# Kernel optimization log

Hardware: AMD Instinct MI355X
Metric: run time of the kernel (lower is better)

Reference implementation:

```python
import jax, jax.numpy as jnp
import numpy as np

B, C, H, W = 4, 64, 256, 256
WS = 8          # window size
HEADS = 4       # dim // dim_head, dim_head = 16
DH = 16         # dim_head used for scale
HID = 64        # gated conv FFN hidden (mult=1)


def conv2d(x, w, b=None, stride=1, pad=1, groups=1):
    out = jax.lax.conv_general_dilated(
        x, w, (stride, stride), [(pad, pad), (pad, pad)],
        feature_group_count=groups,
        dimension_numbers=('NCHW', 'OIHW', 'NCHW'))
    if b is not None:
        out = out + b[None, :, None, None]
    return out


def gelu(x):
    return jax.nn.gelu(x, approximate=False)  # torch F.gelu / nn.GELU default (erf)


def ln2d(x, w, b, eps=1e-6):  # LayerNorm2d: normalize over channel dim
    mu = jnp.mean(x, axis=1, keepdims=True)
    var = jnp.mean((x - mu) ** 2, axis=1, keepdims=True)
    return w[None, :, None, None] * ((x - mu) / jnp.sqrt(var + eps)) + b[None, :, None, None]


def ln_last(x, w, b, eps=1e-5):  # nn.LayerNorm over last dim
    mu = jnp.mean(x, axis=-1, keepdims=True)
    var = jnp.mean((x - mu) ** 2, axis=-1, keepdims=True)
    return w * ((x - mu) / jnp.sqrt(var + eps)) + b


def to_windows(x, w):  # b d (x w1) (y w2) -> b x y w1 w2 d
    b, c, h, ww = x.shape
    x = x.reshape(b, c, h // w, w, ww // w, w)
    return jnp.transpose(x, (0, 2, 4, 3, 5, 1))


def from_windows(x):  # b x y w1 w2 d -> b d (x w1) (y w2)
    b, nx, ny, w1, w2, c = x.shape
    return jnp.transpose(x, (0, 5, 1, 3, 2, 4)).reshape(b, c, nx * w1, ny * w2)


def setup_inputs() -> dict:
    key = jax.random.key(0)
    ks = iter(jax.random.split(key, 64))

    def rn(*shape):
        return jax.random.normal(next(ks), shape, dtype=jnp.float32) * 0.05

    d = dict(
        x=jax.random.normal(next(ks), (B, C, H, W), dtype=jnp.float32),
        norm_w=jnp.ones((C,), jnp.float32), norm_b=jnp.zeros((C,), jnp.float32),
        conv1_w=rn(C, C, 1, 1), conv1_b=jnp.zeros((C,), jnp.float32),
        conv2_w=rn(C, 2 * C, 1, 1), conv2_b=jnp.zeros((C,), jnp.float32),
        mb_w1=rn(C, C, 1, 1), mb_b1=jnp.zeros((C,), jnp.float32),
        mb_dw_w=rn(C, 1, 3, 3), mb_dw_b=jnp.zeros((C,), jnp.float32),
        se_w1=rn(16, C), se_w2=rn(C, 16),
        mb_w2=rn(C, C, 1, 1), mb_b2=jnp.zeros((C,), jnp.float32),
        ln_att_w=jnp.ones((C,), jnp.float32), ln_att_b=jnp.zeros((C,), jnp.float32),
        q1_w=rn(C // 2, C), q1_b=jnp.zeros((C // 2,), jnp.float32),
        qkv_w=rn(3 * C // 2, C // 2),
        to_out_w=rn(C // 2, C // 2),
        sr_w=rn(C, C, 3, 3), sr_b=jnp.zeros((C,), jnp.float32),
        ln_sr_w=jnp.ones((C,), jnp.float32), ln_sr_b=jnp.zeros((C,), jnp.float32),
        kv1_w=rn(C, C), kv1_b=jnp.zeros((C,), jnp.float32),
        q2_w=rn(C // 2, C), q2_b=jnp.zeros((C // 2,), jnp.float32),
        cd_w=rn(C // 2, C // 2, 3, 3), cd_b=jnp.zeros((C // 2,), jnp.float32),
        cu_w=rn(C // 2, C // 2, 3, 3), cu_b=jnp.zeros((C // 2,), jnp.float32),
        cln1_w=jnp.ones((C,), jnp.float32), cln1_b=jnp.zeros((C,), jnp.float32),
        ff1_in_w=rn(2 * HID, C, 1, 1), ff1_dw_w=rn(2 * HID, 1, 3, 3), ff1_out_w=rn(C, HID, 1, 1),
        cln2_w=jnp.ones((C,), jnp.float32), cln2_b=jnp.zeros((C,), jnp.float32),
        ca_temp=jnp.ones((HEADS, 1, 1), jnp.float32),
        ca_qkv_w=rn(3 * C, C, 1, 1), ca_dw_w=rn(3 * C, 1, 3, 3), ca_out_w=rn(C, C, 1, 1),
        cln3_w=jnp.ones((C,), jnp.float32), cln3_b=jnp.zeros((C,), jnp.float32),
        ff2_in_w=rn(2 * HID, C, 1, 1), ff2_dw_w=rn(2 * HID, 1, 3, 3), ff2_out_w=rn(C, HID, 1, 1),
    )
    return d


def reference(x, norm_w, norm_b, conv1_w, conv1_b, conv2_w, conv2_b,
              mb_w1, mb_b1, mb_dw_w, mb_dw_b, se_w1, se_w2, mb_w2, mb_b2,
              ln_att_w, ln_att_b, q1_w, q1_b, qkv_w, to_out_w,
              sr_w, sr_b, ln_sr_w, ln_sr_b, kv1_w, kv1_b, q2_w, q2_b,
              cd_w, cd_b, cu_w, cu_b,
              cln1_w, cln1_b, ff1_in_w, ff1_dw_w, ff1_out_w,
              cln2_w, cln2_b, ca_temp, ca_qkv_w, ca_dw_w, ca_out_w,
              cln3_w, cln3_b, ff2_in_w, ff2_dw_w, ff2_out_w):
    scale = DH ** -0.5
    # input norm + 1x1 conv
    y = conv2d(ln2d(x, norm_w, norm_b), conv1_w, conv1_b, pad=0)
    # ---- MBConv (expansion 1, SE, residual) ----
    r = y
    t = gelu(conv2d(y, mb_w1, mb_b1, pad=0))
    t = gelu(conv2d(t, mb_dw_w, mb_dw_b, pad=1, groups=C))
    s = jnp.mean(t, axis=(2, 3))                      # (B,C) squeeze
    s = jax.nn.sigmoid(jax.nn.silu(s @ se_w1.T) @ se_w2.T)
    y = conv2d(t * s[:, :, None, None], mb_w2, mb_b2, pad=0) + r
    # ---- windowed hybrid attention, PreNormResidual ----
    xw = to_windows(y, WS)                            # (B,nx,ny,8,8,C)
    xn = ln_last(xw, ln_att_w, ln_att_b)
    xf = from_windows(xn)                             # (B,C,H,W)
    b, c, h, w = xf.shape
    nx, ny = h // WS, w // WS
    # window self-attention branch on dim/2
    xq = jnp.einsum('bchw,oc->bohw', xf, q1_w) + q1_b[None, :, None, None]
    tw = to_windows(xq, WS).reshape(b * nx * ny, WS * WS, c // 2)
    qkv = tw @ qkv_w.T
    q, k, v = jnp.split(qkv, 3, axis=-1)

    def heads_split(t):
        return jnp.transpose(t.reshape(t.shape[0], WS * WS, HEADS, -1), (0, 2, 1, 3))

    q, k, v = heads_split(q) * scale, heads_split(k), heads_split(v)
    attn = jax.nn.softmax(jnp.einsum('bhid,bhjd->bhij', q, k), axis=-1)
    o = jnp.einsum('bhij,bhjd->bhid', attn, v)
    o = jnp.transpose(o, (0, 2, 1, 3)).reshape(b * nx * ny, WS, WS, c // 2)
    o = (o @ to_out_w.T).reshape(b, nx, ny, WS, WS, c // 2)
    # low-resolution cross-attention branch on dim/2
    iq = jnp.einsum('bchw,oc->bohw', xf, q2_w) + q2_b[None, :, None, None]
    iq = conv2d(iq, cd_w, cd_b, stride=8, pad=1)      # (B,C/2,H/8,W/8)
    qq = jnp.transpose(iq.reshape(b, h * w // 64, HEADS // 2, c // HEADS), (0, 2, 1, 3))
    x1 = conv2d(xf, sr_w, sr_b, stride=16, pad=1)     # (B,C,h16,w16)
    x1 = jnp.transpose(x1.reshape(b, c, -1), (0, 2, 1))
    x1 = gelu(ln_last(x1, ln_sr_w, ln_sr_b))
    kv = (x1 @ kv1_w.T + kv1_b).reshape(b, -1, 2, HEADS // 2, c // HEADS)
    kv = jnp.transpose(kv, (2, 0, 3, 1, 4))
    k1, v1 = kv[0], kv[1]                             # (B,2,N,16)
    a1 = jax.nn.softmax(jnp.einsum('bhid,bhjd->bhij', qq, k1) * scale, axis=-1)
    o1 = jnp.einsum('bhij,bhjd->bhid', a1, v1)        # (B,2,HW/64,16)
    o1 = jnp.transpose(o1, (0, 1, 3, 2)).reshape(b, c // 2, h // 8, w // 8)
    o1 = jnp.repeat(jnp.repeat(o1, 8, axis=2), 8, axis=3)   # nearest upsample x8
    o1 = to_windows(conv2d(o1, cu_w, cu_b, pad=1), WS)
    xw = jnp.concatenate([o, o1], axis=-1) + xw       # residual
    y = from_windows(xw)

    def gcff(z, in_w, dw_w, out_w):
        t = conv2d(conv2d(z, in_w, pad=0), dw_w, pad=1, groups=2 * HID)
        a, g = jnp.split(t, 2, axis=1)
        return conv2d(gelu(a) * g, out_w, pad=0)

    y = y + gcff(ln2d(y, cln1_w, cln1_b), ff1_in_w, ff1_dw_w, ff1_out_w)
    # ---- windowed channel (transposed) attention ----
    z = ln2d(y, cln2_w, cln2_b)
    qkv2 = conv2d(conv2d(z, ca_qkv_w, pad=0), ca_dw_w, pad=1, groups=3 * C)
    qc, kc, vc = jnp.split(qkv2, 3, axis=1)
    hp, wp = h // WS, w // WS

    def rw(t):  # b (head d) (h ph) (w pw) -> b (h w) head d (ph pw)
        t = t.reshape(b, HEADS, C // HEADS, hp, WS, wp, WS)
        return jnp.transpose(t, (0, 3, 5, 1, 2, 4, 6)).reshape(b, hp * wp, HEADS, C // HEADS, WS * WS)

    qc, kc, vc = rw(qc), rw(kc), rw(vc)
    qc = qc / jnp.clip(jnp.linalg.norm(qc, axis=-1, keepdims=True), 1e-12)
    kc = kc / jnp.clip(jnp.linalg.norm(kc, axis=-1, keepdims=True), 1e-12)
    aat = jax.nn.softmax(jnp.einsum('bnhde,bnhfe->bnhdf', qc, kc) * ca_temp, axis=-1)
    oc = jnp.einsum('bnhdf,bnhfe->bnhde', aat, vc)    # (B,Nw,head,16,64)
    oc = oc.reshape(b, hp, wp, HEADS, C // HEADS, WS, WS)
    oc = jnp.transpose(oc, (0, 3, 4, 1, 5, 2, 6)).reshape(b, C, h, w)
    y = y + conv2d(oc, ca_out_w, pad=0)
    y = y + gcff(ln2d(y, cln3_w, cln3_b), ff2_in_w, ff2_dw_w, ff2_out_w)
    # fuse branch with block input
    return conv2d(jnp.concatenate([x, y], axis=1), conv2_w, conv2_b, pad=0)
```

## Files before the change

### kernel.cpp

```cpp
#include <hip/hip_runtime.h>
#include <hip/hip_bf16.h>
#include <math.h>

typedef __hip_bfloat16 bf16;

static constexpr int B_ = 4;
static constexpr int C_ = 64;
static constexpr int H_ = 256;
static constexpr int W_ = 256;
static constexpr int P_ = H_ * W_;
static constexpr int NP_ = B_ * P_;

static constexpr int HSTR = 61;

__device__ __forceinline__ float cvt(float x) { return x; }
__device__ __forceinline__ float cvt(bf16 x) { return __bfloat162float(x); }
__device__ __forceinline__ float geluf(float x) { return 0.5f * x * (1.0f + erff(x * 0.70710678118654752f)); }
__device__ __forceinline__ float sigm(float x) { return 1.0f / (1.0f + __expf(-x)); }

__device__ __forceinline__ float ldin(const void* p, int i, bool bf) {
    return bf ? __bfloat162float(((const bf16*)p)[i]) : ((const float*)p)[i];
}

__device__ __forceinline__ void bf2x(unsigned u, float& a, float& b) {
// ... 105 lines not shown
    int p = g & (P_ - 1);
    int base = bb * C_ * P_ + p;
    float v[C_];
    float mu = 0.f;
#pragma unroll
    for (int c = 0; c < C_; ++c) { v[c] = in[base + c * P_]; mu += v[c]; }
    mu *= (1.0f / C_);
    float var = 0.f;
#pragma unroll
    for (int c = 0; c < C_; ++c) { float d = v[c] - mu; var += d * d; }
    var *= (1.0f / C_);
    float inv = rsqrtf(var + eps);
#pragma unroll
    for (int c = 0; c < C_; ++c)
        out[base + c * P_] = __float2bfloat16((v[c] - mu) * inv * swt[c] + sbt[c]);
}

template <int COUT>
__global__ __launch_bounds__(256) void k_pwln(const float* __restrict__ Yin,
                                              const void* __restrict__ lnw, const void* __restrict__ lnb,
                                              const void* __restrict__ w,
                                              bf16* __restrict__ out,
                                              const int* __restrict__ dtf) {
    const bool bf = dtf[0] != 0;
    __shared__ bf16 swb[COUT * 64];
    __shared__ float slw[64], slb[64];
    for (int i = threadIdx.x; i < COUT * 64; i += 256) swb[i] = __float2bfloat16(ldin(w, i, bf));
    if (threadIdx.x < 64) {
        slw[threadIdx.x] = ldin(lnw, threadIdx.x, bf);
        slb[threadIdx.x] = ldin(lnb, threadIdx.x, bf);
    }
    __syncthreads();
    int g = blockIdx.x * 256 + threadIdx.x;
    int bb = g >> 16, p = g & (P_ - 1);
    int base = bb * 64 * P_ + p;
    float v[64];
    float mu = 0.f;
#pragma unroll
    for (int c = 0; c < 64; ++c) { v[c] = Yin[base + c * P_]; mu += v[c]; }
    mu *= (1.0f / 64.0f);
    float var = 0.f;
#pragma unroll
    for (int c = 0; c < 64; ++c) { float d = v[c] - mu; var += d * d; }
    float inv = rsqrtf(var * (1.0f / 64.0f) + 1e-6f);
#pragma unroll
    for (int c = 0; c < 64; ++c) v[c] = (v[c] - mu) * inv * slw[c] + slb[c];
    int obase = bb * COUT * P_ + p;
    const unsigned* uw = (const unsigned*)swb;
    for (int o = 0; o < COUT; ++o) {
        float a = 0.f;
#pragma unroll
        for (int cc = 0; cc < 32; ++cc) {
            float wa, wb;
            bf2x(uw[o * 32 + cc], wa, wb);
            a = fmaf(wa, v[2 * cc], fmaf(wb, v[2 * cc + 1], a));
        }
        out[obase + o * P_] = __float2bfloat16(a);
    }
}

__global__ __launch_bounds__(256) void k_dwmean(const bf16* __restrict__ h,
                                                const void* __restrict__ dww,
                                                const void* __restrict__ dwb,
                                                float* __restrict__ part,
                                                const int* __restrict__ dtf) {
    const bool bf = dtf[0] != 0;
    __shared__ __align__(8) bf16 hsb[10 * 256];
    __shared__ float red[256];
    int bid = blockIdx.x;
    int bc = bid >> 5, chunk = bid & 31;
    int c = bc & 63;
    int h0 = chunk * 8;
    int base = bc * P_;
    int tid = threadIdx.x;
    {
        const unsigned* gq = (const unsigned*)h;
        unsigned* hu = (unsigned*)hsb;
        for (int i = tid; i < 1280; i += 256) {
            int r = i >> 7, col2 = i & 127;
            int hh = h0 - 1 + r;
            unsigned v = 0u;
            if ((unsigned)hh < (unsigned)H_) v = gq[(base + hh * W_) / 2 + col2];
            hu[r * 128 + col2] = v;
        }
    }
    float w9[9];
#pragma unroll
    for (int k = 0; k < 9; ++k) w9[k] = ldin(dww, c * 9 + k, bf);
    float bv = ldin(dwb, c, bf);
    __syncthreads();
    float acc = 0.f;
#pragma unroll
    for (int k = 0; k < 8; ++k) {
        int j = tid + k * 256;
        int r = j >> 8, x = j & 255;
        float s = bv;
#pragma unroll
        for (int kh = 0; kh < 3; ++kh) {
            const bf16* row = &hsb[(r + kh) * 256];
            float vm1 = (x > 0) ? cvt(row[x - 1]) : 0.f;
            float v0 = cvt(row[x]);
            float vp1 = (x < 255) ? cvt(row[x + 1]) : 0.f;
            s = fmaf(w9[kh * 3 + 0], vm1, s);
            s = fmaf(w9[kh * 3 + 1], v0, s);
            s = fmaf(w9[kh * 3 + 2], vp1, s);
        }
        acc += geluf(s);
    }
    red[tid] = acc;
    __syncthreads();
    for (int s2 = 128; s2 > 0; s2 >>= 1) {
        if (tid < s2) red[tid] += red[tid + s2];
        __syncthreads();
    }
    if (tid == 0) part[bc * 32 + chunk] = red[0];
}

__global__ __launch_bounds__(256) void k_se(const float* __restrict__ part,
                                            const void* __restrict__ w1,
                                            const void* __restrict__ w2,
                                            float* __restrict__ sfin,
                                            const int* __restrict__ dtf) {
    const bool bf = dtf[0] != 0;
    __shared__ float ssum[256];
    __shared__ float hbuf[B_ * 16];
    int t = threadIdx.x;
    {
        float a = 0.f;
#pragma unroll
        for (int k = 0; k < 32; ++k) a += part[t * 32 + k];
        ssum[t] = a * (1.0f / P_);
    }
    __syncthreads();
    if (t < B_ * 16) {
        int bb = t >> 4, j = t & 15;
        float a = 0.f;
        for (int c = 0; c < 64; ++c) a = fmaf(ssum[bb * 64 + c], ldin(w1, j * 64 + c, bf), a);
        hbuf[t] = a * sigm(a);
    }
    __syncthreads();
    int bb = t >> 6, c = t & 63;
    float a = 0.f;
    for (int j = 0; j < 16; ++j) a = fmaf(hbuf[bb * 16 + j], ldin(w2, c * 16 + j, bf), a);
    sfin[t] = sigm(a);
}

__global__ __launch_bounds__(256) void k_mb2w(const bf16* __restrict__ h,
                                              const void* __restrict__ dww, const void* __restrict__ dwb,
                                              const void* __restrict__ w2, const void* __restrict__ b2,
                                              const float* __restrict__ sfin,
                                              float* __restrict__ Y,
                                              const int* __restrict__ dtf) {
    const bool bf = dtf[0] != 0;
    __shared__ __align__(16) char arena[24832];
    unsigned* hsu = (unsigned*)arena;
    bf16* ts = (bf16*)(arena + 15616);
    float* sdb = (float*)(arena + 24064);
    float* sb2 = (float*)(arena + 24320);
    float* ssc = (float*)(arena + 24576);
    bf16* sw2T = (bf16*)arena;
    int wid = win_swz(blockIdx.x);
    int bb = wid >> 10;
    int h0 = ((wid >> 5) & 31) * 8, w0 = (wid & 31) * 8;
    int tid = threadIdx.x;
    int cch = tid >> 2, quarter = tid & 3;
    {
        const unsigned* gq = (const unsigned*)h;
        int j = quarter * 15;
        int pr = j / 6, col = j - pr * 6;
        size_t chb = (size_t)(bb * 64 + cch) * P_;
        for (int k = 0; k < 15; ++k) {
            int hh = h0 + pr - 1;
            int wcx = w0 - 2 + 2 * col;
            unsigned v = 0u;
            if ((unsigned)hh < (unsigned)H_ && (unsigned)wcx < 255u)
                v = gq[(chb + hh * W_ + wcx) >> 1];
            hsu[cch * HSTR + j] = v;
            ++j; ++col;
            if (col == 6) { col = 0; ++pr; }
        }
    }
    float w9[9];
#pragma unroll
    for (int k = 0; k < 9; ++k) w9[k] = ldin(dww, cch * 9 + k, bf);
    if (tid < 64) {
        sdb[tid] = ldin(dwb, tid, bf);
        sb2[tid] = ldin(b2, tid, bf);
        ssc[tid] = sfin[bb * 64 + tid];
    }
    __syncthreads();
    {
        const unsigned* mua = hsu + cch * HSTR;
        unsigned* tsu = (unsigned*)ts;
        float bv = sdb[cch];
        float sc = ssc[cch];
#pragma unroll
        for (int k = 0; k < 8; ++k) {
            int p = quarter * 8 + k;
            int t0 = 2 * p;
            int rt = t0 >> 3, ct = t0 & 7;
            float a0 = bv, a1 = bv;
#pragma unroll
            for (int kh = 0; kh < 3; ++kh) {
                int rb = (rt + kh) * 6 + (ct >> 1);
                unsigned u0 = mua[rb], u1 = mua[rb + 1], u2 = mua[rb + 2];
                float x1 = bfhi(u0);
                float x2 = bflo(u1), x3 = bfhi(u1);
                float x4 = bflo(u2);
                a0 = fmaf(w9[kh * 3 + 0], x1, fmaf(w9[kh * 3 + 1], x2, fmaf(w9[kh * 3 + 2], x3, a0)));
                a1 = fmaf(w9[kh * 3 + 0], x2, fmaf(w9[kh * 3 + 1], x3, fmaf(w9[kh * 3 + 2], x4, a1)));
            }
            tsu[cch * 33 + p] = bfpack(geluf(a0) * sc, geluf(a1) * sc);
        }
    }
    __syncthreads();
    for (int i = tid; i < 4096; i += 256) {
        int c = i >> 6, o = i & 63;
        sw2T[c * 64 + o] = __float2bfloat16(ldin(w2, o * 64 + c, bf));
    }
    __syncthreads();
    int og = tid >> 4, pg = tid & 15;
    int o0 = og * 4, p0 = pg * 4;
    float acc[4][4] = {};
    const unsigned* wt = (const unsigned*)sw2T;
    const unsigned* tt = (const unsigned*)ts;
    for (int c = 0; c < 64; ++c) {
        float w0v, w1v, w2v, w3v, t0, t1, t2, t3;
        bf2x(wt[c * 32 + (o0 >> 1)], w0v, w1v);
        bf2x(wt[c * 32 + (o0 >> 1) + 1], w2v, w3v);
        bf2x(tt[c * 33 + (p0 >> 1)], t0, t1);
        bf2x(tt[c * 33 + (p0 >> 1) + 1], t2, t3);
        acc[0][0] = fmaf(w0v, t0, acc[0][0]); acc[0][1] = fmaf(w0v, t1, acc[0][1]);
        acc[0][2] = fmaf(w0v, t2, acc[0][2]); acc[0][3] = fmaf(w0v, t3, acc[0][3]);
        acc[1][0] = fmaf(w1v, t0, acc[1][0]); acc[1][1] = fmaf(w1v, t1, acc[1][1]);
        acc[1][2] = fmaf(w1v, t2, acc[1][2]); acc[1][3] = fmaf(w1v, t3, acc[1][3]);
        acc[2][0] = fmaf(w2v, t0, acc[2][0]); acc[2][1] = fmaf(w2v, t1, acc[2][1]);
        acc[2][2] = fmaf(w2v, t2, acc[2][2]); acc[2][3] = fmaf(w2v, t3, acc[2][3]);
        acc[3][0] = fmaf(w3v, t0, acc[3][0]); acc[3][1] = fmaf(w3v, t1, acc[3][1]);
        acc[3][2] = fmaf(w3v, t2, acc[3][2]); acc[3][3] = fmaf(w3v, t3, acc[3][3]);
    }
#pragma unroll
    for (int i = 0; i < 4; ++i)
#pragma unroll
        for (int j = 0; j < 4; ++j) {
            int t = p0 + j;
            int p = (h0 + (t >> 3)) * W_ + w0 + (t & 7);
            Y[(bb * 64 + o0 + i) * P_ + p] += acc[i][j] + sb2[o0 + i];
        }
}

__global__ __launch_bounds__(256) void k_wprep(const void* __restrict__ q1w, const void* __restrict__ q1b,
                                               const void* __restrict__ qkvw, const void* __restrict__ outw,
                                               bf16* __restrict__ WQT, float* __restrict__ BQ,
                                               bf16* __restrict__ OWT,
                                               const int* __restrict__ dtf) {
    const bool bf = dtf[0] != 0;
    __shared__ float sq1[32 * 64];
    __shared__ float sqk[96 * 32];
    __shared__ float sb1[32];
    int tid = threadIdx.x;
    for (int i = tid; i < 2048; i += 256) sq1[i] = ldin(q1w, i, bf);
    for (int i = tid; i < 3072; i += 256) sqk[i] = ldin(qkvw, i, bf);
    if (tid < 32) sb1[tid] = ldin(q1b, tid, bf);
    __syncthreads();
    for (int idx = tid; idx < 6144; idx += 256) {
        int o = idx % 96, c = idx / 96;
        float a = 0.f;
        for (int k = 0; k < 32; ++k) a = fmaf(sqk[o * 32 + k], sq1[k * 64 + c], a);
        if (o < 32) a *= 0.25f;
        WQT[c * 96 + o] = __float2bfloat16(a);
    }
    if (tid < 96) {
        float a = 0.f;
        for (int k = 0; k < 32; ++k) a = fmaf(sqk[tid * 32 + k], sb1[k], a);
        if (tid < 32) a *= 0.25f;
        BQ[tid] = a;
    }
    for (int idx = tid; idx < 1024; idx += 256) {
        int o = idx >> 5, c = idx & 31;
        OWT[c * 32 + o] = __float2bfloat16(ldin(outw, o * 32 + c, bf));
    }
}

__global__ __launch_bounds__(256, 4) void k_winattn(const bf16* __restrict__ xf,
                                                    const uint4* __restrict__ WQT,
                                                    const float* __restrict__ BQ,
                                                    const unsigned* __restrict__ OWT,
                                                    float* __restrict__ Y) {
    __shared__ __align__(16) char arena[35200];
    int wid = win_swz(blockIdx.x);
    int bb = wid >> 10;
    int h0 = ((wid >> 5) & 31) * 8, w0 = (wid & 31) * 8;
    int tid = threadIdx.x;
    {
        uint4* sW4 = (uint4*)arena;
        for (int i = tid; i < 768; i += 256) sW4[i] = WQT[i];
        if (tid < 96) ((float*)(arena + 12288))[tid] = BQ[tid];
#pragma unroll
        for (int k = 0; k < 2; ++k) {
            int idx = tid + k * 256;
            int c = idx >> 3, r = idx & 7;
            const uint4 v = *(const uint4*)(xf + (size_t)(bb * 64 + c) * P_ + (h0 + r) * W_ + w0);
            *(uint4*)(arena + 12672 + c * 144 + r * 16) = v;
        }
    }
    __syncthreads();
    {
        const unsigned* uW = (const unsigned*)arena;
        const float* sbq = (const float*)(arena + 12288);
        const unsigned* uX = (const unsigned*)(arena + 12672);
        unsigned* uQw = (unsigned*)(arena + 21888);
        int og = tid >> 4, pg = tid & 15;
        float acc[6][4];
#pragma unroll
        for (int i = 0; i < 6; ++i) {
            float b = sbq[og * 6 + i];
#pragma unroll
            for (int j = 0; j < 4; ++j) acc[i][j] = b;
        }
        for (int c = 0; c < 64; ++c) {
            unsigned wu0 = uW[c * 48 + 3 * og];
            unsigned wu1 = uW[c * 48 + 3 * og + 1];
            unsigned wu2 = uW[c * 48 + 3 * og + 2];
            unsigned xu0 = uX[c * 36 + 2 * pg];
            unsigned xu1 = uX[c * 36 + 2 * pg + 1];
            float wv[6], xv[4];
            bf2x(wu0, wv[0], wv[1]); bf2x(wu1, wv[2], wv[3]); bf2x(wu2, wv[4], wv[5]);
            bf2x(xu0, xv[0], xv[1]); bf2x(xu1, xv[2], xv[3]);
#pragma unroll
            for (int i = 0; i < 6; ++i)
#pragma unroll
                for (int j = 0; j < 4; ++j) acc[i][j] = fmaf(wv[i], xv[j], acc[i][j]);
        }
#pragma unroll
        for (int j = 0; j < 4; ++j) {
            int t = pg * 4 + j;
#pragma unroll
            for (int k = 0; k < 3; ++k) {
                union { unsigned u; bf16 h[2]; } pk;
                pk.h[0] = __float2bfloat16(acc[2 * k][j]);
                pk.h[1] = __float2bfloat16(acc[2 * k + 1][j]);
                uQw[t * 52 + 3 * og + k] = pk.u;
            }
        }
    }
    __syncthreads();
    {
        int hH = tid >> 6, lane = tid & 63;
        const unsigned* uQ = (const unsigned*)(arena + 21888);
        unsigned ow0 = OWT[tid * 2], ow1 = OWT[tid * 2 + 1];
        float qf[8];
        {
            const uint4 qv = *(const uint4*)&uQ[lane * 52 + hH * 4];
            bf2x(qv.x, qf[0], qf[1]); bf2x(qv.y, qf[2], qf[3]);
            bf2x(qv.z, qf[4], qf[5]); bf2x(qv.w, qf[6], qf[7]);
        }
        float p[64];
#pragma unroll
        for (int j = 0; j < 64; ++j) {
            const uint4 kv4 = *(const uint4*)&uQ[j * 52 + 16 + hH * 4];
            float kf[8];
            bf2x(kv4.x, kf[0], kf[1]); bf2x(kv4.y, kf[2], kf[3]);
            bf2x(kv4.z, kf[4], kf[5]); bf2x(kv4.w, kf[6], kf[7]);
            float s = 0.f;
#pragma unroll
            for (int d = 0; d < 8; ++d) s = fmaf(qf[d], kf[d], s);
            p[j] = s;
        }
        float m0 = fmaxf(p[0], p[4]), m1 = fmaxf(p[1], p[5]);
        float m2 = fmaxf(p[2], p[6]), m3 = fmaxf(p[3], p[7]);
#pragma unroll
// ... 98 lines not shown
    int bb = g / (OS * OS * COUT);
    float acc = ldin(bias, oc, bf);
    for (int ic = 0; ic < CIN; ++ic) {
        int ibase = (bb * CIN + ic) * P_;
        int wbase = (oc * CIN + ic) * 9;
#pragma unroll
        for (int kh = 0; kh < 3; ++kh) {
            int ih = oh * STRIDE + kh - 1;
            if ((unsigned)ih >= (unsigned)H_) continue;
#pragma unroll
            for (int kw = 0; kw < 3; ++kw) {
                int iw = ow * STRIDE + kw - 1;
                if ((unsigned)iw >= (unsigned)W_) continue;
                acc = fmaf(ldin(w, wbase + kh * 3 + kw, bf), cvt(in[ibase + ih * W_ + iw]), acc);
            }
        }
    }
    out[g] = acc;
}

__global__ __launch_bounds__(64) void k_srkv(const float* __restrict__ x1,
                                             const void* __restrict__ lnw,
                                             const void* __restrict__ lnb,
                                             const void* __restrict__ kvw,
                                             const void* __restrict__ kvb,
                                             float* __restrict__ k1,
                                             float* __restrict__ v1,
                                             const int* __restrict__ dtf) {
    const bool bf = dtf[0] != 0;
    int tok = blockIdx.x;
    int bb = tok >> 8;
    int n = tok & 255;
    int c = threadIdx.x;
    __shared__ float sv[64];
    __shared__ float sg[64];
    float v = x1[(bb * 64 + c) * 256 + n];
    sv[c] = v;
    __syncthreads();
    float mu = 0.f;
    for (int i = 0; i < 64; ++i) mu += sv[i];
    mu *= (1.0f / 64.0f);
    float var = 0.f;
    for (int i = 0; i < 64; ++i) { float d = sv[i] - mu; var += d * d; }
    var *= (1.0f / 64.0f);
    float xn = (v - mu) * rsqrtf(var + 1e-5f) * ldin(lnw, c, bf) + ldin(lnb, c, bf);
    sg[c] = geluf(xn);
    __syncthreads();
    float acc = ldin(kvb, c, bf);
    for (int j = 0; j < 64; ++j) acc = fmaf(ldin(kvw, c * 64 + j, bf), sg[j], acc);
    int kk = c >> 5;
    int jh = (c >> 4) & 1;
    int d = c & 15;
    float* dst = kk ? v1 : k1;
    dst[((bb * 2 + jh) * 256 + n) * 16 + d] = acc;
}

__global__ __launch_bounds__(256) void k_xattn(const float* __restrict__ iqd,
                                               const float* __restrict__ k1,
                                               const float* __restrict__ v1,
                                               float* __restrict__ o1sp) {
    int bid = blockIdx.x;
    int iblk = bid & 3;
    int j = (bid >> 2) & 1;
    int bb = bid >> 3;
    __shared__ float sk[256 * 16];
    __shared__ float svv[256 * 16];
    int kbase = ((bb * 2 + j) * 256) * 16;
    for (int idx = threadIdx.x; idx < 4096; idx += 256) { sk[idx] = k1[kbase + idx]; svv[idx] = v1[kbase + idx]; }
    __syncthreads();
    int i = iblk * 256 + threadIdx.x;
    float q[16];
    int qbase = ((bb * 32 + (i >> 5)) * 32 + (i & 31)) * 32 + j * 16;
#pragma unroll
    for (int d = 0; d < 16; ++d) q[d] = iqd[qbase + d];
    float m = -1e30f, l = 0.f, o[16];
#pragma unroll
    for (int d = 0; d < 16; ++d) o[d] = 0.f;
    for (int n = 0; n < 256; ++n) {
        float s = 0.f;
#pragma unroll
        for (int d = 0; d < 16; ++d) s = fmaf(q[d], sk[n * 16 + d], s);
        s *= 0.25f;
        float mn = fmaxf(m, s);
        float corr = __expf(m - mn);
        float e = __expf(s - mn);
        l = l * corr + e;
#pragma unroll
        for (int d = 0; d < 16; ++d) o[d] = fmaf(o[d], corr, e * svv[n * 16 + d]);
        m = mn;
    }
    float r = 1.0f / l;
#pragma unroll
    for (int d = 0; d < 16; ++d)
        o1sp[((bb * 32 + j * 16 + d) * 32 + (i >> 5)) * 32 + (i & 31)] = o[d] * r;
}

__global__ __launch_bounds__(256) void k_cuconv(const float* __restrict__ o1sp,
                                                const void* __restrict__ w,
                                                const void* __restrict__ bias,
                                                float* __restrict__ Y,
                                                const int* __restrict__ dtf) {
    const bool bf = dtf[0] != 0;
    __shared__ float sw[32 * 32 * 9];
    for (int i = threadIdx.x; i < 9216; i += 256) sw[i] = ldin(w, i, bf);
    __syncthreads();
    int g = blockIdx.x * 256 + threadIdx.x;
    int bb = g >> 16;
    int p = g & 65535;
    int h = p >> 8, x = p & 255;
    float acc[32];
#pragma unroll
    for (int oc = 0; oc < 32; ++oc) acc[oc] = ldin(bias, oc, bf);
    for (int ic = 0; ic < 32; ++ic) {
        int ibase = (bb * 32 + ic) * 1024;
        float v[9];
#pragma unroll
        for (int kh = 0; kh < 3; ++kh)
#pragma unroll
            for (int kw = 0; kw < 3; ++kw) {
                int hh = h + kh - 1, ww = x + kw - 1;
                v[kh * 3 + kw] = ((unsigned)hh < (unsigned)H_ && (unsigned)ww < (unsigned)W_)
                                     ? o1sp[ibase + (hh >> 3) * 32 + (ww >> 3)] : 0.f;
            }
        for (int oc = 0; oc < 32; ++oc) {
            const float* wr = &sw[(oc * 32 + ic) * 9];
            float a = acc[oc];
#pragma unroll
            for (int k = 0; k < 9; ++k) a = fmaf(wr[k], v[k], a);
            acc[oc] = a;
        }
    }
#pragma unroll
    for (int oc = 0; oc < 32; ++oc) Y[(bb * 64 + 32 + oc) * P_ + p] += acc[oc];
}

__global__ __launch_bounds__(256) void k_gcff2(const bf16* __restrict__ mid_g,
                                               const void* __restrict__ dww,
                                               const void* __restrict__ outw,
                                               float* __restrict__ Y,
                                               const int* __restrict__ dtf) {
    const bool bf = dtf[0] != 0;
    __shared__ __align__(16) char arena[24064];
    unsigned* cbu = (unsigned*)arena;
    bf16* ts = (bf16*)(arena + 15616);
    bf16* sowT = (bf16*)arena;
    int wid = win_swz(blockIdx.x);
    int bb = wid >> 10;
    int h0 = ((wid >> 5) & 31) * 8, w0 = (wid & 31) * 8;
    int tid = threadIdx.x;
    int cch = tid >> 2, quarter = tid & 3;
    int j0 = quarter * 15;
    int pr0 = j0 / 6, col0 = j0 - pr0 * 6;
    const unsigned* gq = (const unsigned*)mid_g;
    float areg[16];
    float w9[9];
    {
        int j = j0, pr = pr0, col = col0;
        size_t chb = (size_t)(bb * 128 + cch) * P_;
        for (int k = 0; k < 15; ++k) {
            int hh = h0 + pr - 1;
            int wcx = w0 - 2 + 2 * col;
            unsigned v = 0u;
            if ((unsigned)hh < (unsigned)H_ && (unsigned)wcx < 255u)
                v = gq[(chb + hh * W_ + wcx) >> 1];
            cbu[cch * HSTR + j] = v;
            ++j; ++col;
            if (col == 6) { col = 0; ++pr; }
        }
    }
#pragma unroll
    for (int k = 0; k < 9; ++k) w9[k] = ldin(dww, cch * 9 + k, bf);
    __syncthreads();
    {
        const unsigned* mua = cbu + cch * HSTR;
#pragma unroll
        for (int k = 0; k < 8; ++k) {
            int p = quarter * 8 + k;
            int t0 = 2 * p;
            int rt = t0 >> 3, ct = t0 & 7;
            float a0 = 0.f, a1 = 0.f;
#pragma unroll
            for (int kh = 0; kh < 3; ++kh) {
                int rb = (rt + kh) * 6 + (ct >> 1);
                unsigned u0 = mua[rb], u1 = mua[rb + 1], u2 = mua[rb + 2];
                float x1 = bfhi(u0);
                float x2 = bflo(u1), x3 = bfhi(u1);
                float x4 = bflo(u2);
                a0 = fmaf(w9[kh * 3 + 0], x1, fmaf(w9[kh * 3 + 1], x2, fmaf(w9[kh * 3 + 2], x3, a0)));
                a1 = fmaf(w9[kh * 3 + 0], x2, fmaf(w9[kh * 3 + 1], x3, fmaf(w9[kh * 3 + 2], x4, a1)));
            }
            areg[2 * k] = a0;
            areg[2 * k + 1] = a1;
        }
    }
    __syncthreads();
    {
        int j = j0, pr = pr0, col = col0;
        size_t chb = (size_t)(bb * 128 + 64 + cch) * P_;
        for (int k = 0; k < 15; ++k) {
            int hh = h0 + pr - 1;
            int wcx = w0 - 2 + 2 * col;
            unsigned v = 0u;
            if ((unsigned)hh < (unsigned)H_ && (unsigned)wcx < 255u)
                v = gq[(chb + hh * W_ + wcx) >> 1];
            cbu[cch * HSTR + j] = v;
            ++j; ++col;
            if (col == 6) { col = 0; ++pr; }
        }
    }
#pragma unroll
    for (int k = 0; k < 9; ++k) w9[k] = ldin(dww, (64 + cch) * 9 + k, bf);
    __syncthreads();
    {
        const unsigned* mua = cbu + cch * HSTR;
        unsigned* tsu = (unsigned*)ts;
#pragma unroll
        for (int k = 0; k < 8; ++k) {
            int p = quarter * 8 + k;
            int t0 = 2 * p;
            int rt = t0 >> 3, ct = t0 & 7;
            float g0 = 0.f, g1 = 0.f;
#pragma unroll
            for (int kh = 0; kh < 3; ++kh) {
                int rb = (rt + kh) * 6 + (ct >> 1);
                unsigned u0 = mua[rb], u1 = mua[rb + 1], u2 = mua[rb + 2];
                float x1 = bfhi(u0);
                float x2 = bflo(u1), x3 = bfhi(u1);
                float x4 = bflo(u2);
                g0 = fmaf(w9[kh * 3 + 0], x1, fmaf(w9[kh * 3 + 1], x2, fmaf(w9[kh * 3 + 2], x3, g0)));
                g1 = fmaf(w9[kh * 3 + 0], x2, fmaf(w9[kh * 3 + 1], x3, fmaf(w9[kh * 3 + 2], x4, g1)));
            }
            tsu[cch * 33 + p] = bfpack(geluf(areg[2 * k]) * g0, geluf(areg[2 * k + 1]) * g1);
        }
    }
    __syncthreads();
    for (int i = tid; i < 4096; i += 256) {
        int c = i >> 6, o = i & 63;
        sowT[c * 64 + o] = __float2bfloat16(ldin(outw, o * 64 + c, bf));
    }
    __syncthreads();
    int og = tid >> 4, pg = tid & 15;
    int o0 = og * 4, p0 = pg * 4;
    float acc[4][4] = {};
    const unsigned* wt = (const unsigned*)sowT;
    const unsigned* tt = (const unsigned*)ts;
    for (int c = 0; c < 64; ++c) {
        float w0v, w1v, w2v, w3v, t0, t1, t2, t3;
        bf2x(wt[c * 32 + (o0 >> 1)], w0v, w1v);
        bf2x(wt[c * 32 + (o0 >> 1) + 1], w2v, w3v);
        bf2x(tt[c * 33 + (p0 >> 1)], t0, t1);
        bf2x(tt[c * 33 + (p0 >> 1) + 1], t2, t3);
        acc[0][0] = fmaf(w0v, t0, acc[0][0]); acc[0][1] = fmaf(w0v, t1, acc[0][1]);
        acc[0][2] = fmaf(w0v, t2, acc[0][2]); acc[0][3] = fmaf(w0v, t3, acc[0][3]);
        acc[1][0] = fmaf(w1v, t0, acc[1][0]); acc[1][1] = fmaf(w1v, t1, acc[1][1]);
        acc[1][2] = fmaf(w1v, t2, acc[1][2]); acc[1][3] = fmaf(w1v, t3, acc[1][3]);
        acc[2][0] = fmaf(w2v, t0, acc[2][0]); acc[2][1] = fmaf(w2v, t1, acc[2][1]);
        acc[2][2] = fmaf(w2v, t2, acc[2][2]); acc[2][3] = fmaf(w2v, t3, acc[2][3]);
        acc[3][0] = fmaf(w3v, t0, acc[3][0]); acc[3][1] = fmaf(w3v, t1, acc[3][1]);
        acc[3][2] = fmaf(w3v, t2, acc[3][2]); acc[3][3] = fmaf(w3v, t3, acc[3][3]);
    }
#pragma unroll
    for (int i = 0; i < 4; ++i)
#pragma unroll
        for (int j = 0; j < 4; ++j) {
            int t = p0 + j;
            int p = (h0 + (t >> 3)) * W_ + w0 + (t & 7);
            Y[(bb * 64 + o0 + i) * P_ + p] += acc[i][j];
        }
}

__global__ __launch_bounds__(256) void k_chattn2(const bf16* __restrict__ qkv_g,
                                                 const void* __restrict__ dww,
                                                 const void* __restrict__ outw,
                                                 const void* __restrict__ tempw,
                                                 float* __restrict__ Y,
                                                 const int* __restrict__ dtf) {
    const bool bf = dtf[0] != 0;
    __shared__ __align__(16) char arena[40960];
    bf16* sq = (bf16*)arena;
    bf16* chunkb = (bf16*)(arena + 25344);
    bf16* s_owT = (bf16*)arena;
    float* s_att = (float*)(arena + 25344);
    bf16* s_oc = (bf16*)(arena + 29696);
    int wid = win_swz(blockIdx.x);
    int bb = wid >> 10;
    int h0 = ((wid >> 5) & 31) * 8, w0 = (wid & 31) * 8;
    int tid = threadIdx.x;
    int cch = tid >> 2, quarter = tid & 3;
    const unsigned* gq = (const unsigned*)qkv_g;
    unsigned* cbu = (unsigned*)chunkb;
    unsigned* squ = (unsigned*)sq;
    int j0 = quarter * 15;
    int pr0 = j0 / 6, col0 = j0 - pr0 * 6;
    for (int chunk = 0; chunk < 3; ++chunk) {
        int ch0 = chunk * 64;
        {
            int j = j0, pr = pr0, col = col0;
            size_t chb = (size_t)((bb * 192 + ch0 + cch) * P_);
            for (int k = 0; k < 15; ++k) {
                int hh = h0 + pr - 1;
                int wcx = w0 - 2 + 2 * col;
                unsigned v = 0u;
                if ((unsigned)hh < (unsigned)H_ && (unsigned)wcx < 255u)
                    v = gq[(chb + hh * W_ + wcx) >> 1];
                cbu[cch * HSTR + j] = v;
                ++j; ++col;
                if (col == 6) { col = 0; ++pr; }
            }
        }
        float w9[9];
#pragma unroll
        for (int k = 0; k < 9; ++k) w9[k] = ldin(dww, (ch0 + cch) * 9 + k, bf);
        __syncthreads();
        {
            const unsigned* mua = cbu + cch * HSTR;
#pragma unroll
            for (int k = 0; k < 8; ++k) {
                int p = quarter * 8 + k;
                int t0 = 2 * p;
                int rt = t0 >> 3, ct = t0 & 7;
                float a0 = 0.f, a1 = 0.f;
#pragma unroll
                for (int kh = 0; kh < 3; ++kh) {
                    int rb = (rt + kh) * 6 + (ct >> 1);
                    unsigned u0 = mua[rb], u1 = mua[rb + 1], u2 = mua[rb + 2];
                    float x1 = bfhi(u0);
                    float x2 = bflo(u1), x3 = bfhi(u1);
                    float x4 = bflo(u2);
                    a0 = fmaf(w9[kh * 3 + 0], x1, fmaf(w9[kh * 3 + 1], x2, fmaf(w9[kh * 3 + 2], x3, a0)));
                    a1 = fmaf(w9[kh * 3 + 0], x2, fmaf(w9[kh * 3 + 1], x3, fmaf(w9[kh * 3 + 2], x4, a1)));
                }
                squ[(ch0 + cch) * 33 + p] = bfpack(a0, a1);
            }
        }
        __syncthreads();
    }
    if (tid < 128) {
        unsigned* row = squ + tid * 33;
        float v[64];
        float ss = 0.f;
#pragma unroll
        for (int t2 = 0; t2 < 32; ++t2) {
            bf2x(row[t2], v[2 * t2], v[2 * t2 + 1]);
            ss = fmaf(v[2 * t2], v[2 * t2], fmaf(v[2 * t2 + 1], v[2 * t2 + 1], ss));
        }
        float inv = 1.0f / fmaxf(sqrtf(ss), 1e-12f);
#pragma unroll
        for (int t2 = 0; t2 < 32; ++t2)
            row[t2] = bfpack(v[2 * t2] * inv, v[2 * t2 + 1] * inv);
    }
    __syncthreads();
    for (int i = tid; i < 1024; i += 256) {
        int hh = i >> 8, d = (i >> 4) & 15, f = i & 15;
        const unsigned* qrow = squ + (hh * 16 + d) * 33;
        const unsigned* krow = squ + (64 + hh * 16 + f) * 33;
        float acc = 0.f;
#pragma unroll
        for (int t2 = 0; t2 < 32; ++t2) {
            float q0, q1, k0, k1;
            bf2x(qrow[t2], q0, q1);
            bf2x(krow[t2], k0, k1);
            acc = fmaf(q0, k0, fmaf(q1, k1, acc));
        }
        s_att[(hh * 16 + d) * 17 + f] = acc * ldin(tempw, hh, bf);
    }
    __syncthreads();
    if (tid < 64) {
        int row = tid;
        float m = -1e30f;
        for (int f = 0; f < 16; ++f) m = fmaxf(m, s_att[row * 17 + f]);
        float sum = 0.f;
        for (int f = 0; f < 16; ++f) { float e = __expf(s_att[row * 17 + f] - m); s_att[row * 17 + f] = e; sum += e; }
        float r = 1.0f / sum;
        for (int f = 0; f < 16; ++f) s_att[row * 17 + f] *= r;
    }
    __syncthreads();
    {
        unsigned* s_ocu = (unsigned*)s_oc;
        for (int i = tid; i < 2048; i += 256) {
            int row = i >> 5, p = i & 31;
            int hh = row >> 4, d = row & 15;
            const float* arow = &s_att[(hh * 16 + d) * 17];
            float o0 = 0.f, o1 = 0.f;
#pragma unroll
            for (int f = 0; f < 16; ++f) {
                float av = arow[f];
                float v0, v1;
                bf2x(squ[(128 + hh * 16 + f) * 33 + p], v0, v1);
                o0 = fmaf(av, v0, o0);
                o1 = fmaf(av, v1, o1);
            }
            s_ocu[row * 33 + p] = bfpack(o0, o1);
        }
        for (int i = tid; i < 4096; i += 256) {
            int c = i >> 6, o = i & 63;
            s_owT[c * 64 + o] = __float2bfloat16(ldin(outw, o * 64 + c, bf));
        }
    }
    __syncthreads();
    int og = tid >> 4, pg = tid & 15;
    int o0 = og * 4, p0 = pg * 4;
    float acc[4][4] = {};
    const unsigned* wt = (const unsigned*)s_owT;
    const unsigned* tt = (const unsigned*)s_oc;
    for (int c = 0; c < 64; ++c) {
        float w0v, w1v, w2v, w3v, t0, t1, t2, t3;
        bf2x(wt[c * 32 + (o0 >> 1)], w0v, w1v);
        bf2x(wt[c * 32 + (o0 >> 1) + 1], w2v, w3v);
        bf2x(tt[c * 33 + (p0 >> 1)], t0, t1);
        bf2x(tt[c * 33 + (p0 >> 1) + 1], t2, t3);
        acc[0][0] = fmaf(w0v, t0, acc[0][0]); acc[0][1] = fmaf(w0v, t1, acc[0][1]);
        acc[0][2] = fmaf(w0v, t2, acc[0][2]); acc[0][3] = fmaf(w0v, t3, acc[0][3]);
        acc[1][0] = fmaf(w1v, t0, acc[1][0]); acc[1][1] = fmaf(w1v, t1, acc[1][1]);
        acc[1][2] = fmaf(w1v, t2, acc[1][2]); acc[1][3] = fmaf(w1v, t3, acc[1][3]);
        acc[2][0] = fmaf(w2v, t0, acc[2][0]); acc[2][1] = fmaf(w2v, t1, acc[2][1]);
        acc[2][2] = fmaf(w2v, t2, acc[2][2]); acc[2][3] = fmaf(w2v, t3, acc[2][3]);
        acc[3][0] = fmaf(w3v, t0, acc[3][0]); acc[3][1] = fmaf(w3v, t1, acc[3][1]);
        acc[3][2] = fmaf(w3v, t2, acc[3][2]); acc[3][3] = fmaf(w3v, t3, acc[3][3]);
    }
#pragma unroll
    for (int i = 0; i < 4; ++i)
#pragma unroll
        for (int j = 0; j < 4; ++j) {
            int t = p0 + j;
            int p = (h0 + (t >> 3)) * W_ + w0 + (t & 7);
            Y[(bb * 64 + o0 + i) * P_ + p] += acc[i][j];
        }
}

__global__ __launch_bounds__(256) void k_final(const void* __restrict__ x,
                                               const float* __restrict__ Yb,
                                               const void* __restrict__ w,
                                               const void* __restrict__ bias,
                                               void* __restrict__ out,
                                               const int* __restrict__ dtf) {
    const bool bf = dtf[0] != 0;
    __shared__ float sw[64 * 128];
    __shared__ float sb[64];
    for (int i = threadIdx.x; i < 8192; i += 256) sw[i] = ldin(w, i, bf);
    if (threadIdx.x < 64) sb[threadIdx.x] = ldin(bias, threadIdx.x, bf);
    __syncthreads();
    int g = blockIdx.x * 256 + threadIdx.x;
    int bb = g >> 16;
    int p = g & 65535;
    float xv[64], yv[64];
    int base = bb * 64 * P_ + p;
#pragma unroll
    for (int c = 0; c < 64; ++c) xv[c] = ldin(x, base + c * P_, bf);
#pragma unroll
    for (int c = 0; c < 64; ++c) yv[c] = Yb[base + c * P_];
    for (int o = 0; o < 64; ++o) {
        float acc = sb[o];
        const float* wr = &sw[o * 128];
#pragma unroll
        for (int c = 0; c < 64; ++c) acc = fmaf(wr[c], xv[c], acc);
#pragma unroll
        for (int c = 0; c < 64; ++c) acc = fmaf(wr[64 + c], yv[c], acc);
        if (bf) ((bf16*)out)[base + o * P_] = __float2bfloat16(acc);
        else    ((float*)out)[base + o * P_] = acc;
    }
}

extern "C" void kernel_launch(void* const* d_in, const int* in_sizes, int n_in,
                              void* d_out, int out_size, void* d_ws, size_t ws_size,
                              hipStream_t stream) {
    const void* x        = d_in[0];
    const void* norm_w   = d_in[1];
    const void* norm_b   = d_in[2];
    const void* conv1_w  = d_in[3];
    const void* conv1_b  = d_in[4];
    const void* conv2_w  = d_in[5];
    const void* conv2_b  = d_in[6];
    const void* mb_w1    = d_in[7];
    const void* mb_b1    = d_in[8];
    const void* mb_dw_w  = d_in[9];
    const void* mb_dw_b  = d_in[10];
    const void* se_w1    = d_in[11];
    const void* se_w2    = d_in[12];
    const void* mb_w2    = d_in[13];
    const void* mb_b2    = d_in[14];
    const void* ln_att_w = d_in[15];
    const void* ln_att_b = d_in[16];
    const void* q1_w     = d_in[17];
    const void* q1_b     = d_in[18];
    const void* qkv_w    = d_in[19];
    const void* to_out_w = d_in[20];
    const void* sr_w     = d_in[21];
    const void* sr_b     = d_in[22];
    const void* ln_sr_w  = d_in[23];
    const void* ln_sr_b  = d_in[24];
    const void* kv1_w    = d_in[25];
    const void* kv1_b    = d_in[26];
    const void* q2_w     = d_in[27];
    const void* q2_b     = d_in[28];
    const void* cd_w     = d_in[29];
    const void* cd_b     = d_in[30];
    const void* cu_w     = d_in[31];
    const void* cu_b     = d_in[32];
    const void* cln1_w   = d_in[33];
    const void* cln1_b   = d_in[34];
    const void* ff1_in_w = d_in[35];
    const void* ff1_dw_w = d_in[36];
    const void* ff1_out_w= d_in[37];
    const void* cln2_w   = d_in[38];
// ... 57 lines not shown
```

Before: 2.240 ms.

## Prefetch next channel chunk into registers and fuse L2 normalization into depthwise pass

The windowed attention and gated FFN kernels now load the next 64-channel halo chunk into registers while the current chunk's depthwise conv runs, overlapping global loads with compute. The attention kernel also computes the q/k L2 norms with a warp shuffle inside the depthwise loop, which removes a separate normalization pass and one barrier. In the MBConv kernel the shared arena is split into separate buffers, so the w2 transpose can be staged before the first barrier and one sync is dropped. The cost is higher register use (15 prefetch registers plus 16 values) and more shared memory in k_mb2w, which may lower occupancy.

```diff
diff --git a/kernel.cpp b/kernel.cpp
--- a/kernel.cpp
+++ b/kernel.cpp
@@ -281,13 +281,10 @@
                                               float* __restrict__ Y,
                                               const int* __restrict__ dtf) {
     const bool bf = dtf[0] != 0;
-    __shared__ __align__(16) char arena[24832];
-    unsigned* hsu = (unsigned*)arena;
-    bf16* ts = (bf16*)(arena + 15616);
-    float* sdb = (float*)(arena + 24064);
-    float* sb2 = (float*)(arena + 24320);
-    float* ssc = (float*)(arena + 24576);
-    bf16* sw2T = (bf16*)arena;
+    __shared__ __align__(16) bf16 hs[64 * 2 * HSTR];
+    __shared__ __align__(16) bf16 ts[64 * 66];
+    __shared__ __align__(16) bf16 sw2T[64 * 64];
+    __shared__ float sdb[64], sb2[64], ssc[64];
     int wid = win_swz(blockIdx.x);
     int bb = wid >> 10;
     int h0 = ((wid >> 5) & 31) * 8, w0 = (wid & 31) * 8;
@@ -295,6 +292,7 @@
     int cch = tid >> 2, quarter = tid & 3;
     {
         const unsigned* gq = (const unsigned*)h;
+        unsigned* hsu = (unsigned*)hs;
         int j = quarter * 15;
         int pr = j / 6, col = j - pr * 6;
         size_t chb = (size_t)(bb * 64 + cch) * P_;
@@ -312,6 +310,10 @@
     float w9[9];
 #pragma unroll
     for (int k = 0; k < 9; ++k) w9[k] = ldin(dww, cch * 9 + k, bf);
+    for (int i = tid; i < 4096; i += 256) {
+        int c = i >> 6, o = i & 63;
+        sw2T[c * 64 + o] = __float2bfloat16(ldin(w2, o * 64 + c, bf));
+    }
     if (tid < 64) {
         sdb[tid] = ldin(dwb, tid, bf);
         sb2[tid] = ldin(b2, tid, bf);
@@ -319,7 +321,7 @@
     }
     __syncthreads();
     {
-        const unsigned* mua = hsu + cch * HSTR;
+        const unsigned* mua = (const unsigned*)hs + cch * HSTR;
         unsigned* tsu = (unsigned*)ts;
         float bv = sdb[cch];
         float sc = ssc[cch];
@@ -341,11 +343,6 @@
             }
             tsu[cch * 33 + p] = bfpack(geluf(a0) * sc, geluf(a1) * sc);
         }
-    }
-    __syncthreads();
-    for (int i = tid; i < 4096; i += 256) {
-        int c = i >> 6, o = i & 63;
-        sw2T[c * 64 + o] = __float2bfloat16(ldin(w2, o * 64 + c, bf));
     }
     __syncthreads();
     int og = tid >> 4, pg = tid & 15;
@@ -750,25 +747,42 @@
     int j0 = quarter * 15;
     int pr0 = j0 / 6, col0 = j0 - pr0 * 6;
     const unsigned* gq = (const unsigned*)mid_g;
+    unsigned regs[15];
     float areg[16];
     float w9[9];
     {
-        int j = j0, pr = pr0, col = col0;
+        int pr = pr0, col = col0;
         size_t chb = (size_t)(bb * 128 + cch) * P_;
+#pragma unroll
         for (int k = 0; k < 15; ++k) {
             int hh = h0 + pr - 1;
             int wcx = w0 - 2 + 2 * col;
             unsigned v = 0u;
             if ((unsigned)hh < (unsigned)H_ && (unsigned)wcx < 255u)
                 v = gq[(chb + hh * W_ + wcx) >> 1];
-            cbu[cch * HSTR + j] = v;
-            ++j; ++col;
-            if (col == 6) { col = 0; ++pr; }
-        }
-    }
+            regs[k] = v;
+            ++col; if (col == 6) { col = 0; ++pr; }
+        }
+    }
+#pragma unroll
+    for (int k = 0; k < 15; ++k) cbu[cch * HSTR + j0 + k] = regs[k];
 #pragma unroll
     for (int k = 0; k < 9; ++k) w9[k] = ldin(dww, cch * 9 + k, bf);
     __syncthreads();
+    {
+        int pr = pr0, col = col0;
+        size_t chb = (size_t)(bb * 128 + 64 + cch) * P_;
+#pragma unroll
+        for (int k = 0; k < 15; ++k) {
+            int hh = h0 + pr - 1;
+            int wcx = w0 - 2 + 2 * col;
+            unsigned v = 0u;
+            if ((unsigned)hh < (unsigned)H_ && (unsigned)wcx < 255u)
+                v = gq[(chb + hh * W_ + wcx) >> 1];
+            regs[k] = v;
+            ++col; if (col == 6) { col = 0; ++pr; }
+        }
+    }
     {
         const unsigned* mua = cbu + cch * HSTR;
 #pragma unroll
@@ -792,20 +806,8 @@
         }
     }
     __syncthreads();
-    {
-        int j = j0, pr = pr0, col = col0;
-        size_t chb = (size_t)(bb * 128 + 64 + cch) * P_;
-        for (int k = 0; k < 15; ++k) {
-            int hh = h0 + pr - 1;
-            int wcx = w0 - 2 + 2 * col;
-            unsigned v = 0u;
-            if ((unsigned)hh < (unsigned)H_ && (unsigned)wcx < 255u)
-                v = gq[(chb + hh * W_ + wcx) >> 1];
-            cbu[cch * HSTR + j] = v;
-            ++j; ++col;
-            if (col == 6) { col = 0; ++pr; }
-        }
-    }
+#pragma unroll
+    for (int k = 0; k < 15; ++k) cbu[cch * HSTR + j0 + k] = regs[k];
 #pragma unroll
     for (int k = 0; k < 9; ++k) w9[k] = ldin(dww, (64 + cch) * 9 + k, bf);
     __syncthreads();
@@ -890,28 +892,47 @@
     unsigned* squ = (unsigned*)sq;
     int j0 = quarter * 15;
     int pr0 = j0 / 6, col0 = j0 - pr0 * 6;
+    unsigned regs[15];
+    {
+        int pr = pr0, col = col0;
+        size_t chb = (size_t)((bb * 192 + cch) * P_);
+#pragma unroll
+        for (int k = 0; k < 15; ++k) {
+            int hh = h0 + pr - 1;
+            int wcx = w0 - 2 + 2 * col;
+            unsigned v = 0u;
+            if ((unsigned)hh < (unsigned)H_ && (unsigned)wcx < 255u)
+                v = gq[(chb + hh * W_ + wcx) >> 1];
+            regs[k] = v;
+            ++col; if (col == 6) { col = 0; ++pr; }
+        }
+    }
     for (int chunk = 0; chunk < 3; ++chunk) {
         int ch0 = chunk * 64;
-        {
-            int j = j0, pr = pr0, col = col0;
-            size_t chb = (size_t)((bb * 192 + ch0 + cch) * P_);
+#pragma unroll
+        for (int k = 0; k < 15; ++k) cbu[cch * HSTR + j0 + k] = regs[k];
+        float w9[9];
+#pragma unroll
+        for (int k = 0; k < 9; ++k) w9[k] = ldin(dww, (ch0 + cch) * 9 + k, bf);
+        __syncthreads();
+        if (chunk < 2) {
+            int pr = pr0, col = col0;
+            size_t chb = (size_t)((bb * 192 + ch0 + 64 + cch) * P_);
+#pragma unroll
             for (int k = 0; k < 15; ++k) {
                 int hh = h0 + pr - 1;
                 int wcx = w0 - 2 + 2 * col;
                 unsigned v = 0u;
                 if ((unsigned)hh < (unsigned)H_ && (unsigned)wcx < 255u)
                     v = gq[(chb + hh * W_ + wcx) >> 1];
-                cbu[cch * HSTR + j] = v;
-                ++j; ++col;
-                if (col == 6) { col = 0; ++pr; }
+                regs[k] = v;
+                ++col; if (col == 6) { col = 0; ++pr; }
             }
         }
-        float w9[9];
-#pragma unroll
-        for (int k = 0; k < 9; ++k) w9[k] = ldin(dww, (ch0 + cch) * 9 + k, bf);
-        __syncthreads();
         {
             const unsigned* mua = cbu + cch * HSTR;
+            float vals[16];
+            float ss = 0.f;
 #pragma unroll
             for (int k = 0; k < 8; ++k) {
                 int p = quarter * 8 + k;
@@ -928,26 +949,22 @@
                     a0 = fmaf(w9[kh * 3 + 0], x1, fmaf(w9[kh * 3 + 1], x2, fmaf(w9[kh * 3 + 2], x3, a0)));
                     a1 = fmaf(w9[kh * 3 + 0], x2, fmaf(w9[kh * 3 + 1], x3, fmaf(w9[kh * 3 + 2], x4, a1)));
                 }
-                squ[(ch0 + cch) * 33 + p] = bfpack(a0, a1);
+                vals[2 * k] = a0; vals[2 * k + 1] = a1;
+                ss = fmaf(a0, a0, fmaf(a1, a1, ss));
             }
+            if (chunk < 2) {
+                ss += __shfl_xor(ss, 1);
+                ss += __shfl_xor(ss, 2);
+                float inv = 1.0f / fmaxf(sqrtf(ss), 1e-12f);
+#pragma unroll
+                for (int k = 0; k < 16; ++k) vals[k] *= inv;
+            }
+#pragma unroll
+            for (int k = 0; k < 8; ++k)
+                squ[(ch0 + cch) * 33 + quarter * 8 + k] = bfpack(vals[2 * k], vals[2 * k + 1]);
         }
         __syncthreads();
     }
-    if (tid < 128) {
-        unsigned* row = squ + tid * 33;
-        float v[64];
-        float ss = 0.f;
-#pragma unroll
-        for (int t2 = 0; t2 < 32; ++t2) {
-            bf2x(row[t2], v[2 * t2], v[2 * t2 + 1]);
-            ss = fmaf(v[2 * t2], v[2 * t2], fmaf(v[2 * t2 + 1], v[2 * t2 + 1], ss));
-        }
-        float inv = 1.0f / fmaxf(sqrtf(ss), 1e-12f);
-#pragma unroll
-        for (int t2 = 0; t2 < 32; ++t2)
-            row[t2] = bfpack(v[2 * t2] * inv, v[2 * t2 + 1] * inv);
-    }
-    __syncthreads();
     for (int i = tid; i < 1024; i += 256) {
         int hh = i >> 8, d = (i >> 4) & 15, f = i & 15;
         const unsigned* qrow = squ + (hh * 16 + d) * 33;
```

Result: faster. 2.140 ms (-4.5%).
